# Kernel optimization log

Measured on AMD Instinct MI355X. Metric: run time of the kernel, lower is better.

The kernel has to match this reference:

```python
import jax, jax.numpy as jnp
import numpy as np

SIGMA = 25.0
EPS = 1e-5
TWO_PI = 2.0 * np.pi


def _gn(x, gamma, beta, groups):
    # GroupNorm over (C//G, H, W) per group, per-channel affine.
    B, C, H, W = x.shape
    xg = x.reshape(B, groups, -1)
    m = xg.mean(-1, keepdims=True)
    v = xg.var(-1, keepdims=True)
    xn = ((xg - m) * jax.lax.rsqrt(v + EPS)).reshape(B, C, H, W)
    return xn * gamma[None, :, None, None] + beta[None, :, None, None]


def _conv3(x, k, b):
    y = jax.lax.conv_general_dilated(x, k, (1, 1), 'SAME',
                                     dimension_numbers=('NCHW', 'OIHW', 'NCHW'))
    return y + b[None, :, None, None]


def _tconv2(x, k, b):
    # ConvTranspose2d kernel=2 stride=2 (no overlap) == einsum + reshape.
    # k: [C_in, C_out, 2, 2]
    B, C, H, W = x.shape
    O = k.shape[1]
    y = jnp.einsum('bchw,codq->bohdwq', x, k).reshape(B, O, 2 * H, 2 * W)
    return y + b[None, :, None, None]


def _conv1(x, k, b):
    # 1x1 conv; k: [C_out, C_in]
    return jnp.einsum('bchw,oc->bohw', x, k) + b[None, :, None, None]


def _pool(x):
    B, C, H, W = x.shape
    return x.reshape(B, C, H // 2, 2, W // 2, 2).max(axis=(3, 5))


def _std(t):
    return jnp.sqrt((SIGMA ** (2.0 * t) - 1.0) / (2.0 * jnp.log(SIGMA)))


def setup_inputs() -> dict:
    key = jax.random.key(0)
    ks = jax.random.split(key, 16)
    B, H, W = 64, 128, 128
    E = 2 * W  # 256 = embed_dim

    def w(k, shape, fan_in):
        return jax.random.normal(k, shape, jnp.float32) / np.sqrt(fan_in)

    inp = {
        'x': jax.random.normal(ks[0], (B, 1, H, W), jnp.float32),
        't': jax.random.uniform(ks[1], (B,), jnp.float32, 1e-3, 1.0),
        'Wf': jax.random.normal(ks[2], (H, W), jnp.float32) * 30.0,  # fixed Fourier features
        'fc1_w': w(ks[3], (E, E), E),
        'fc1_b': jnp.zeros((E,), jnp.float32),
        'conv1_k': w(ks[4], (6, 1, 3, 3), 9),
        'conv1_b': jnp.zeros((6,), jnp.float32),
        'gn1_g': jnp.ones((6,), jnp.float32), 'gn1_b': jnp.zeros((6,), jnp.float32),
        'conv2_k': w(ks[5], (24, 6, 3, 3), 6 * 9),
        'conv2_b': jnp.zeros((24,), jnp.float32),
        'gn2_g': jnp.ones((24,), jnp.float32), 'gn2_b': jnp.zeros((24,), jnp.float32),
        't3_k': w(ks[6], (24, 24, 2, 2), 24 * 4),
        't3_b': jnp.zeros((24,), jnp.float32),
        'gn3_g': jnp.ones((48,), jnp.float32), 'gn3_b': jnp.zeros((48,), jnp.float32),
        't4_k': w(ks[7], (48, 12, 2, 2), 48 * 4),
        't4_b': jnp.zeros((12,), jnp.float32),
        'gn4_g': jnp.ones((18,), jnp.float32), 'gn4_b': jnp.zeros((18,), jnp.float32),
        't5_k': w(ks[8], (6, 18), 18),
        't5_b': jnp.zeros((6,), jnp.float32),
        'gn5_g': jnp.ones((6,), jnp.float32), 'gn5_b': jnp.zeros((6,), jnp.float32),
        'fin_k': w(ks[9], (1, 6), 6),
        'fin_b': jnp.zeros((1,), jnp.float32),
    }
    return inp


def reference(x, t, Wf, fc1_w, fc1_b, conv1_k, conv1_b, gn1_g, gn1_b,
              conv2_k, conv2_b, gn2_g, gn2_b, t3_k, t3_b, gn3_g, gn3_b,
              t4_k, t4_b, gn4_g, gn4_b, t5_k, t5_b, gn5_g, gn5_b,
              fin_k, fin_b):
    # Vectorized Gaussian Fourier projection: [B,1,H,W] -> [B,1,H,2W]
    p = x * Wf[None, None] * TWO_PI
    xe = jnp.concatenate([jnp.sin(p), jnp.cos(p)], axis=-1)
    # fc1 on last dim (embed_dim = 2W)
    xf = jnp.einsum('bchw,ow->bcho', xe, fc1_w) + fc1_b
    c1 = _conv3(xf, conv1_k, conv1_b)                              # [B,6,H,2W]
    p1 = _pool(jax.nn.relu(_gn(c1, gn1_g, gn1_b, 6)))              # [B,6,H/2,W]
    c2 = _conv3(p1, conv2_k, conv2_b)                              # [B,24,H/2,W]
    p2 = _pool(jax.nn.relu(_gn(c2, gn2_g, gn2_b, 24)))             # [B,24,H/4,W/2]
    a = p2 * jax.nn.sigmoid(p2)                                    # SiLU bottleneck
    u3 = _tconv2(a, t3_k, t3_b)                                    # [B,24,H/2,W]
    g3 = _gn(jnp.concatenate([c2, u3], axis=1), gn3_g, gn3_b, 6)   # 48 ch
    u4 = _tconv2(g3, t4_k, t4_b)                                   # [B,12,H,2W]
    g4 = _gn(jnp.concatenate([c1, u4], axis=1), gn4_g, gn4_b, 6)   # 18 ch
    u5 = _conv1(g4, t5_k, t5_b)                                    # [B,6,H,2W]
    g5 = _gn(u5, gn5_g, gn5_b, 6)
    return _conv1(g5, fin_k, fin_b) / _std(t)[:, None, None, None]
```

## Files before the change

### kernel.cpp

```cpp
#include <hip/hip_runtime.h>
#include <hip/hip_bf16.h>
#include <math.h>

#define BB 64
#define HH 128
#define WW 128
#define EE 256
#define HP (HH*EE)
#define H2 64
#define W2 128
#define PL2 (H2*W2)
#define H4 32
#define W4 64
#define PL4 (H4*W4)

typedef __hip_bfloat16 bf;
typedef unsigned short ushortt;
typedef __attribute__((ext_vector_type(8))) __bf16 b8v;
typedef __attribute__((ext_vector_type(4))) float f4v;

__device__ __forceinline__ float tof(bf v)    { return __bfloat162float(v); }
__device__ __forceinline__ bf    tob(float v) { return __float2bfloat16(v); }
__device__ __forceinline__ unsigned int bfbits(float v) {
    return (unsigned int)__builtin_bit_cast(ushortt, __float2bfloat16(v));
}
__device__ __forceinline__ float b2f(unsigned int u16) {
    unsigned int x = u16 << 16;
    return __builtin_bit_cast(float, x);
}
__device__ __forceinline__ void wred2(float& s, float& q) {
    #pragma unroll
    for (int m = 32; m; m >>= 1) {
        s += __shfl_xor(s, m);
        q += __shfl_xor(q, m);
    }
}

__global__ __launch_bounds__(256) void k_fourier_fc1(
    const float* __restrict__ x, const float* __restrict__ Wf,
    const float* __restrict__ fc1_w, const float* __restrict__ fc1_b,
    bf* __restrict__ xf, float* __restrict__ mb)
{
    __shared__ ushortt sA[64*264];
    __shared__ ushortt sB[64*264];
    int t = threadIdx.x;
    for (int i = blockIdx.x*256 + t; i < 9280; i += 512*256) mb[i] = 0.f;
    int rb = blockIdx.x >> 2, cb = blockIdx.x & 3;
    int row0 = rb*64, col0 = cb*64;
    const float TP = 6.2831853071795864769f;
    for (int it = 0; it < 32; ++it) {
        int i = it*256 + t;
        int r = i >> 7, w = i & 127;
        int rg = row0 + r;
        float p = x[(size_t)rg*WW + w] * Wf[(size_t)(rg & (HH-1))*WW + w] * TP;
        sA[r*264 + w]       = (ushortt)bfbits(__sinf(p));
        sA[r*264 + 128 + w] = (ushortt)bfbits(__cosf(p));
    }
    #pragma unroll
    for (int it = 0; it < 16; ++it) {
        int i = it*256 + t;
        int o = i >> 6, c4 = i & 63;
        float4 w4 = *(const float4*)(fc1_w + (size_t)(col0 + o)*EE + c4*4);
        uint2 pk;
        pk.x = bfbits(w4.x) | (bfbits(w4.y) << 16);
        pk.y = bfbits(w4.z) | (bfbits(w4.w) << 16);
        *(uint2*)&sB[o*264 + c4*4] = pk;
    }
    __syncthreads();
    int lane = t & 63, wid = t >> 6;
    int m = lane & 15, kq = (lane >> 4) * 8;
    f4v acc[4] = {};
    const ushortt* aBase = &sA[(wid*16 + m)*264 + kq];
    #pragma unroll
    for (int k0 = 0; k0 < 8; ++k0) {
        b8v av = *(const b8v*)(aBase + k0*32);
        #pragma unroll
        for (int t4 = 0; t4 < 4; ++t4) {
            b8v bv = *(const b8v*)&sB[(t4*16 + m)*264 + k0*32 + kq];
            acc[t4] = __builtin_amdgcn_mfma_f32_16x16x32_bf16(av, bv, acc[t4], 0, 0, 0);
        }
    }
    int rbase = row0 + wid*16 + (lane >> 4)*4;
    #pragma unroll
    for (int t4 = 0; t4 < 4; ++t4) {
        int col = col0 + t4*16 + m;
        float bias = fc1_b[col];
        #pragma unroll
        for (int r = 0; r < 4; ++r)
            xf[(size_t)(rbase + r)*EE + col] = tob(acc[t4][r] + bias);
    }
}

__global__ __launch_bounds__(256) void k_conv1(
    const bf* __restrict__ xf, const float* __restrict__ k,
    const float* __restrict__ bias, bf* __restrict__ c1, float* __restrict__ mc1)
{
    __shared__ ushortt sT[6*272];
    __shared__ float red[4][6][2];
    int t = threadIdx.x;
    int bid = ((blockIdx.x & 7) << 8) | (blockIdx.x >> 3);
    int ht = bid & 31, b = bid >> 5;
    int h0 = ht*4;
    const bf* src = xf + (size_t)b*HP;
    if (t < 192) {
        int r = t >> 5, i = t & 31;
        int gy = h0 - 1 + r;
        uint4 v = {0,0,0,0};
        if (gy >= 0 && gy < HH) v = *(const uint4*)(src + (size_t)gy*EE + i*8);
        *(uint4*)&sT[r*272 + 8 + i*8] = v;
    } else if (t < 204) {
        int e = t - 192;
        int r = e >> 1, s = e & 1;
        uint4 z = {0,0,0,0};
        *(uint4*)&sT[r*272 + s*264] = z;
    }
    __syncthreads();
    int wq = (t & 63)*4, hl = t >> 6;
    int lane = t & 63, wid = t >> 6;
    float v[3][6];
    #pragma unroll
    for (int ky = 0; ky < 3; ++ky)
      #pragma unroll
      for (int j = 0; j < 6; ++j)
        v[ky][j] = b2f((unsigned)sT[(hl+ky)*272 + 7 + wq + j]);
    int h = h0 + hl;
    #pragma unroll
    for (int o = 0; o < 6; ++o) {
        float bv = bias[o];
        float a0=bv, a1=bv, a2=bv, a3=bv;
        #pragma unroll
        for (int ky = 0; ky < 3; ++ky)
          #pragma unroll
          for (int kx = 0; kx < 3; ++kx) {
            float wv = k[o*9 + ky*3 + kx];
            a0 += v[ky][kx+0]*wv;
            a1 += v[ky][kx+1]*wv;
            a2 += v[ky][kx+2]*wv;
            a3 += v[ky][kx+3]*wv;
          }
        uint2 pk;
        pk.x = bfbits(a0) | (bfbits(a1) << 16);
        pk.y = bfbits(a2) | (bfbits(a3) << 16);
        *(uint2*)(c1 + ((size_t)(b*6+o)*HH + h)*EE + wq) = pk;
        float s = a0+a1+a2+a3, q = a0*a0+a1*a1+a2*a2+a3*a3;
        wred2(s, q);
        if (lane == 0) { red[wid][o][0] = s; red[wid][o][1] = q; }
    }
    __syncthreads();
    if (t < 6) {
        float S = 0.f, Q = 0.f;
        #pragma unroll
        for (int wv = 0; wv < 4; ++wv) { S += red[wv][t][0]; Q += red[wv][t][1]; }
        atomicAdd(&mc1[((size_t)b*6 + t)*2],     S);
        atomicAdd(&mc1[((size_t)b*6 + t)*2 + 1], Q);
    }
}

__global__ __launch_bounds__(256) void k_conv2(
    const bf* __restrict__ c1, const float* __restrict__ mc1,
    const float* __restrict__ g1, const float* __restrict__ be1,
    const float* __restrict__ kw, const float* __restrict__ bias,
    bf* __restrict__ c2, float* __restrict__ mc2)
{
    __shared__ ushortt sA[256*64];
    __shared__ ushortt sW[32*64];
    __shared__ ushortt sP[6*4*136];
    __shared__ float ssl[12];
    __shared__ float redS[24], redQ[24];
    int t = threadIdx.x;
    int bid = ((blockIdx.x & 7) << 8) | (blockIdx.x >> 3);
    int ht = bid & 31, b = bid >> 5;
    int h0 = ht*2;
    int lane = t & 63, wid = t >> 6;
    int m = lane & 15, q4 = lane >> 4;
    if (t < 24) { redS[t] = 0.f; redQ[t] = 0.f; }
    if (t < 6) {
        float s = mc1[((size_t)b*6 + t)*2], q = mc1[((size_t)b*6 + t)*2 + 1];
        float mean = s * (1.f/HP);
        float var  = q * (1.f/HP) - mean*mean;
        float rstd = rsqrtf(var + 1e-5f);
        float sc = g1[t]*rstd;
        ssl[t*2] = sc; ssl[t*2+1] = be1[t] - mean*sc;
    }
    for (int i = t; i < 1024; i += 256) ((unsigned*)sW)[i] = 0;
    if (t < 48) {
        int c = t >> 3, e = t & 7;
        int ry = e >> 1, rx = (e & 1) ? 129 : 0;
        sP[c*544 + ry*136 + rx] = 0;
    }
    __syncthreads();
    #pragma unroll
    for (int j = 0; j < 12; ++j) {
        int i = j*256 + t;
        int c = i >> 9, ry = (i >> 7) & 3, gx = i & 127;
        int gy = h0 - 1 + ry;
        float v = 0.f;
        if (gy >= 0 && gy < H2) {
            const bf* pp = c1 + ((size_t)(b*6+c)*HH + 2*gy)*EE + 2*gx;
            unsigned r0 = *(const unsigned*)pp;
            unsigned r1 = *(const unsigned*)(pp + EE);
            float sc = ssl[c*2], sh = ssl[c*2+1];
            float e0 = fmaxf(b2f(r0 & 0xffff)*sc+sh, 0.f);
            float e1 = fmaxf(b2f(r0 >> 16)   *sc+sh, 0.f);
            float e2 = fmaxf(b2f(r1 & 0xffff)*sc+sh, 0.f);
            float e3 = fmaxf(b2f(r1 >> 16)   *sc+sh, 0.f);
            v = fmaxf(fmaxf(e0,e1), fmaxf(e2,e3));
        }
        sP[c*544 + ry*136 + gx + 1] = (ushortt)bfbits(v);
    }
    #pragma unroll
    for (int j = 0; j < 6; ++j) {
        int i = j*256 + t;
        int o = i >> 6, kk = i & 63;
        if (kk < 54)
            sW[o*64 + ((((kk >> 3) ^ (o & 7)) << 3) | (kk & 7))] =
                (ushortt)bfbits(kw[o*54 + kk]);
    }
    __syncthreads();
    {
        int r = t >> 7, xx = t & 127;
        unsigned u[32];
        #pragma unroll
        for (int p = 0; p < 27; ++p) {
            int k0 = 2*p, k1 = 2*p + 1;
            int c0 = k0/9, y0 = (k0%9)/3, x0 = k0%3;
            int c1i = k1/9, y1 = (k1%9)/3, x1 = k1%3;
            unsigned lo = sP[c0*544 + (r+y0)*136 + xx + x0];
            unsigned hi = sP[c1i*544 + (r+y1)*136 + xx + x1];
            u[p] = lo | (hi << 16);
        }
        #pragma unroll
        for (int p = 27; p < 32; ++p) u[p] = 0;
        #pragma unroll
        for (int e = 0; e < 8; ++e) {
            uint4 pk; pk.x = u[4*e]; pk.y = u[4*e+1]; pk.z = u[4*e+2]; pk.w = u[4*e+3];
            *(uint4*)&sA[t*64 + ((e ^ (t & 7)) << 3)] = pk;
        }
    }
    __syncthreads();
    b8v wv[2][2];
    #pragma unroll
    for (int nt = 0; nt < 2; ++nt) {
        int o = nt*16 + m;
        #pragma unroll
        for (int ks = 0; ks < 2; ++ks)
            wv[nt][ks] = *(const b8v*)&sW[o*64 + (((ks*4 + q4) ^ (o & 7)) << 3)];
    }
    f4v acc[4][2] = {};
    #pragma unroll
    for (int mt = 0; mt < 4; ++mt) {
        int px = wid*64 + mt*16 + m;
        b8v a0 = *(const b8v*)&sA[px*64 + (((q4)     ^ (px & 7)) << 3)];
        b8v a1 = *(const b8v*)&sA[px*64 + (((4 + q4) ^ (px & 7)) << 3)];
        #pragma unroll
        for (int nt = 0; nt < 2; ++nt) {
            acc[mt][nt] = __builtin_amdgcn_mfma_f32_16x16x32_bf16(a0, wv[nt][0], acc[mt][nt], 0, 0, 0);
            acc[mt][nt] = __builtin_amdgcn_mfma_f32_16x16x32_bf16(a1, wv[nt][1], acc[mt][nt], 0, 0, 0);
        }
    }
    float sAcc[2] = {0.f, 0.f}, qAcc[2] = {0.f, 0.f};
    #pragma unroll
    for (int nt = 0; nt < 2; ++nt) {
        int o = nt*16 + m;
        bool valid = (o < 24);
        float bo = valid ? bias[o] : 0.f;
        #pragma unroll
        for (int mt = 0; mt < 4; ++mt) {
            int pxb = wid*64 + mt*16 + q4*4;
            unsigned l0 = bfbits(acc[mt][nt][0] + bo);
            unsigned l1 = bfbits(acc[mt][nt][1] + bo);
            unsigned l2 = bfbits(acc[mt][nt][2] + bo);
            unsigned l3 = bfbits(acc[mt][nt][3] + bo);
            if (valid) {
                uint2 pk; pk.x = l0 | (l1 << 16); pk.y = l2 | (l3 << 16);
                int r = pxb >> 7, xx = pxb & 127;
                *(uint2*)(c2 + ((size_t)(b*24+o))*PL2 + (size_t)(h0 + r)*W2 + xx) = pk;
                float f0 = b2f(l0), f1 = b2f(l1), f2 = b2f(l2), f3 = b2f(l3);
                sAcc[nt] += f0+f1+f2+f3;
                qAcc[nt] += f0*f0+f1*f1+f2*f2+f3*f3;
            }
        }
    }
    #pragma unroll
    for (int nt = 0; nt < 2; ++nt) {
        int o = nt*16 + m;
        float s = sAcc[nt], q = qAcc[nt];
        s += __shfl_xor(s, 16); q += __shfl_xor(q, 16);
        s += __shfl_xor(s, 32); q += __shfl_xor(q, 32);
        if (q4 == 0 && o < 24) { atomicAdd(&redS[o], s); atomicAdd(&redQ[o], q); }
    }
    __syncthreads();
    if (t < 24) {
        atomicAdd(&mc2[((size_t)b*24 + t)*2],     redS[t]);
        atomicAdd(&mc2[((size_t)b*24 + t)*2 + 1], redQ[t]);
    }
}

__global__ __launch_bounds__(256) void k_tconv3(
    const bf* __restrict__ c2, const float* __restrict__ mc2,
    const float* __restrict__ g2, const float* __restrict__ be2,
    const float* __restrict__ k3, const float* __restrict__ b3,
    bf* __restrict__ u3, float* __restrict__ mu3)
{
    __shared__ ushortt sA[128*64];
    __shared__ ushortt sW[96*64];
    __shared__ float redS[24], redQ[24];
    __shared__ float ssl[48];
    int t = threadIdx.x;
    int b = blockIdx.x >> 4, pg = blockIdx.x & 15;
    int lane = t & 63, wid = t >> 6;
    int m = lane & 15, q4 = lane >> 4;
    if (t < 24) {
        redS[t] = 0.f; redQ[t] = 0.f;
        float s = mc2[((size_t)b*24 + t)*2], q = mc2[((size_t)b*24 + t)*2 + 1];
        float mean = s * (1.f/PL2);
        float var  = q * (1.f/PL2) - mean*mean;
        float rstd = rsqrtf(var + 1e-5f);
        float sc = g2[t]*rstd;
        ssl[t*2] = sc; ssl[t*2+1] = be2[t] - mean*sc;
    }
    if (t < 96) {
        uint4 z = {0,0,0,0};
        *(uint4*)&sW[t*64 + (((3 ^ (t & 3)) + (t & 4)) << 3)] = z;
    }
    #pragma unroll
    for (int j = 0; j < 12; ++j) {
        int i = j*256 + t;
        int c = i >> 7, n = i & 127;
        if (n < 96)
            sW[n*64 + (((((c >> 3) ^ (n & 3)) + (n & 4)) << 3) | (c & 7))] =
                (ushortt)bfbits(k3[c*96 + n]);
    }
    {
        int px = t & 127, half = t >> 7;
        int pix = pg*128 + px;
        int h4 = pix >> 6, w4 = pix & 63;
        const bf* base = c2 + (size_t)b*24*PL2 + (size_t)(2*h4)*W2 + 2*w4;
        auto stageG = [&](int g) {
            unsigned pr[4];
            #pragma unroll
            for (int hc = 0; hc < 4; ++hc) {
                unsigned two[2];
                #pragma unroll
                for (int cc = 0; cc < 2; ++cc) {
                    int c = g*8 + hc*2 + cc;
                    const bf* pp = base + (size_t)c*PL2;
                    unsigned r0 = *(const unsigned*)pp;
                    unsigned r1 = *(const unsigned*)(pp + W2);
                    float sc = ssl[c*2], sh = ssl[c*2+1];
                    float e0 = fmaxf(b2f(r0 & 0xffff)*sc+sh, 0.f);
                    float e1 = fmaxf(b2f(r0 >> 16)   *sc+sh, 0.f);
                    float e2 = fmaxf(b2f(r1 & 0xffff)*sc+sh, 0.f);
                    float e3 = fmaxf(b2f(r1 >> 16)   *sc+sh, 0.f);
                    float mm = fmaxf(fmaxf(e0,e1), fmaxf(e2,e3));
                    mm = mm / (1.f + __expf(-mm));
                    two[cc] = bfbits(mm);
                }
                pr[hc] = two[0] | (two[1] << 16);
            }
            uint4 pk; pk.x = pr[0]; pk.y = pr[1]; pk.z = pr[2]; pk.w = pr[3];
            *(uint4*)&sA[px*64 + (((g ^ (px & 3)) + (px & 4)) << 3)] = pk;
        };
        if (half == 0) {
            stageG(0);
            stageG(1);
        } else {
            stageG(2);
            uint4 z = {0,0,0,0};
            *(uint4*)&sA[px*64 + (((3 ^ (px & 3)) + (px & 4)) << 3)] = z;
        }
    }
    __syncthreads();
    b8v wv[6];
    #pragma unroll
    for (int nt = 0; nt < 6; ++nt) {
        int n = nt*16 + m;
        wv[nt] = *(const b8v*)&sW[n*64 + (((q4 ^ (n & 3)) + (n & 4)) << 3)];
    }
    f4v acc[2][6] = {};
    #pragma unroll
    for (int mt = 0; mt < 2; ++mt) {
        int px = wid*32 + mt*16 + m;
        b8v av = *(const b8v*)&sA[px*64 + (((q4 ^ (px & 3)) + (px & 4)) << 3)];
        #pragma unroll
        for (int nt = 0; nt < 6; ++nt)
            acc[mt][nt] = __builtin_amdgcn_mfma_f32_16x16x32_bf16(av, wv[nt], acc[mt][nt], 0, 0, 0);
    }
    float sAcc[6] = {}, qAcc[6] = {};
    int qq = m & 1;
    #pragma unroll
    for (int nt = 0; nt < 6; ++nt) {
        int n = nt*16 + m;
        int o = n >> 2, d = (n >> 1) & 1;
        float bo = b3[o];
        #pragma unroll
        for (int mt = 0; mt < 2; ++mt) {
            int pxb = wid*32 + mt*16 + q4*4;
            unsigned wds[4];
            float s = 0.f, q = 0.f;
            #pragma unroll
            for (int r = 0; r < 4; ++r) {
                float v = acc[mt][nt][r] + bo;
                float vp = __shfl_xor(v, 1);
                unsigned lo = bfbits(v), hi = bfbits(vp);
                wds[r] = lo | (hi << 16);
                float f0 = b2f(lo), f1 = b2f(hi);
                s += f0 + f1;
                q += f0*f0 + f1*f1;
            }
            if (qq == 0) {
                int pix = pg*128 + pxb;
                int h4 = pix >> 6;
                int w4 = pix & 63;
                uint4 pk; pk.x = wds[0]; pk.y = wds[1]; pk.z = wds[2]; pk.w = wds[3];
                *(uint4*)(u3 + ((size_t)(b*24 + o))*PL2 + (size_t)(2*h4 + d)*W2 + 2*w4) = pk;
                sAcc[nt] += s; qAcc[nt] += q;
            }
        }
    }
    #pragma unroll
    for (int nt = 0; nt < 6; ++nt) {
        float s = sAcc[nt], q = qAcc[nt];
        s += __shfl_xor(s, 2);  q += __shfl_xor(q, 2);
        s += __shfl_xor(s, 16); q += __shfl_xor(q, 16);
        s += __shfl_xor(s, 32); q += __shfl_xor(q, 32);
        if ((lane & 51) == 0) {
            int o = nt*4 + (m >> 2);
            atomicAdd(&redS[o], s);
            atomicAdd(&redQ[o], q);
        }
    }
    __syncthreads();
    if (t < 24) {
        atomicAdd(&mu3[((size_t)b*24 + t)*2],     redS[t]);
        atomicAdd(&mu3[((size_t)b*24 + t)*2 + 1], redQ[t]);
    }
}

__global__ __launch_bounds__(256) void k_tconv4(
    const bf* __restrict__ c2, const bf* __restrict__ u3,
    const float* __restrict__ mc2, const float* __restrict__ mu3,
    const float* __restrict__ g3, const float* __restrict__ be3,
    const float* __restrict__ k4, const float* __restrict__ bias4,
    bf* __restrict__ u4, float* __restrict__ mu4)
{
    __shared__ ushortt sA[256*64];
    __shared__ ushortt sW[48*64];
    __shared__ float redS[12], redQ[12];
    __shared__ float ssl[96];
    int t = threadIdx.x;
    int b = blockIdx.x >> 5, pg = blockIdx.x & 31;
    int lane = t & 63, wid = t >> 6;
    int m = lane & 15, q4 = lane >> 4;
    if (t < 12) { redS[t] = 0.f; redQ[t] = 0.f; }
    if (t < 6) {
        float s = 0.f, q = 0.f;
        #pragma unroll
        for (int cl = 0; cl < 8; ++cl) {
            int gc = t*8 + cl;
            const float* p = (gc < 24) ? mc2 + ((size_t)b*24 + gc)*2
                                       : mu3 + ((size_t)b*24 + gc - 24)*2;
            s += p[0]; q += p[1];
        }
        float inv_n = 1.f/((float)PL2*8.f);
        float mean = s*inv_n;
        float var  = q*inv_n - mean*mean;
        float rstd = rsqrtf(var + 1e-5f);
        #pragma unroll
        for (int cl = 0; cl < 8; ++cl) {
            int gc = t*8 + cl;
            float sc = g3[gc]*rstd;
            ssl[gc*2] = sc; ssl[gc*2+1] = be3[gc] - mean*sc;
        }
    }
    #pragma unroll
    for (int j = 0; j < 12; ++j) {
        int i = j*256 + t;
        int c = i >> 6, n = i & 63;
        if (n < 48)
            sW[n*64 + ((((c >> 3) ^ (n & 7)) << 3) | (c & 7))] =
                (ushortt)bfbits(k4[c*48 + n]);
    }
    if (t < 96) {
        uint4 z = {0,0,0,0};
        int n = t >> 1, kb = 6 + (t & 1);
        *(uint4*)&sW[n*64 + ((kb ^ (n & 7)) << 3)] = z;
    }
    {
        int px = t;
        int pix = pg*256 + px;
        const bf* c2p = c2 + (size_t)b*24*PL2 + pix;
        const bf* u3p = u3 + (size_t)b*24*PL2 + pix;
        #pragma unroll
        for (int g = 0; g < 6; ++g) {
            unsigned pr[4];
            #pragma unroll
            for (int hc = 0; hc < 4; ++hc) {
                int c0 = g*8 + hc*2;
                float r0 = (c0 < 24) ? tof(c2p[(size_t)c0*PL2]) : tof(u3p[(size_t)(c0-24)*PL2]);
                float r1 = (c0+1 < 24) ? tof(c2p[(size_t)(c0+1)*PL2]) : tof(u3p[(size_t)(c0+1-24)*PL2]);
                float v0 = r0 * ssl[2*c0]   + ssl[2*c0+1];
                float v1 = r1 * ssl[2*c0+2] + ssl[2*c0+3];
                pr[hc] = bfbits(v0) | (bfbits(v1) << 16);
            }
            uint4 pk; pk.x = pr[0]; pk.y = pr[1]; pk.z = pr[2]; pk.w = pr[3];
            *(uint4*)&sA[px*64 + ((g ^ (px & 7)) << 3)] = pk;
        }
        uint4 z = {0,0,0,0};
        *(uint4*)&sA[px*64 + ((6 ^ (px & 7)) << 3)] = z;
        *(uint4*)&sA[px*64 + ((7 ^ (px & 7)) << 3)] = z;
    }
    __syncthreads();
    b8v bfr[3][2];
    #pragma unroll
    for (int nt = 0; nt < 3; ++nt) {
        int n = nt*16 + m;
        #pragma unroll
        for (int ks = 0; ks < 2; ++ks)
            bfr[nt][ks] = *(const b8v*)&sW[n*64 + (((ks*4 + q4) ^ (n & 7)) << 3)];
    }
    f4v acc[4][3] = {};
    #pragma unroll
    for (int mt = 0; mt < 4; ++mt) {
        int px = wid*64 + mt*16 + m;
        b8v a0 = *(const b8v*)&sA[px*64 + (((q4)     ^ (px & 7)) << 3)];
        b8v a1 = *(const b8v*)&sA[px*64 + (((4 + q4) ^ (px & 7)) << 3)];
        #pragma unroll
        for (int nt = 0; nt < 3; ++nt) {
            acc[mt][nt] = __builtin_amdgcn_mfma_f32_16x16x32_bf16(a0, bfr[nt][0], acc[mt][nt], 0, 0, 0);
            acc[mt][nt] = __builtin_amdgcn_mfma_f32_16x16x32_bf16(a1, bfr[nt][1], acc[mt][nt], 0, 0, 0);
        }
    }
    float sAcc[3] = {0.f, 0.f, 0.f}, qAcc[3] = {0.f, 0.f, 0.f};
    int qq = m & 1;
    #pragma unroll
    for (int nt = 0; nt < 3; ++nt) {
        int n = nt*16 + m;
        int o = n >> 2, d = (n >> 1) & 1;
        float bo = bias4[o];
        #pragma unroll
        for (int mt = 0; mt < 4; ++mt) {
            int pxb = wid*64 + mt*16 + q4*4;
            unsigned wds[4];
            float s = 0.f, q = 0.f;
            #pragma unroll
            for (int r = 0; r < 4; ++r) {
                float v = acc[mt][nt][r] + bo;
                float vp = __shfl_xor(v, 1);
                unsigned lo = bfbits(v), hi = bfbits(vp);
                wds[r] = lo | (hi << 16);
                float f0 = b2f(lo), f1 = b2f(hi);
                s += f0 + f1;
                q += f0*f0 + f1*f1;
            }
            if (qq == 0) {
                int h2 = (pg*256 + pxb) >> 7;
                int w0 = pxb & 127;
                uint4 pk; pk.x = wds[0]; pk.y = wds[1]; pk.z = wds[2]; pk.w = wds[3];
                *(uint4*)(u4 + (((size_t)(b*12 + o))*HH + 2*h2 + d)*EE + 2*w0) = pk;
                sAcc[nt] += s; qAcc[nt] += q;
            }
        }
    }
    #pragma unroll
    for (int nt = 0; nt < 3; ++nt) {
        float s = sAcc[nt], q = qAcc[nt];
        s += __shfl_xor(s, 2);  q += __shfl_xor(q, 2);
        s += __shfl_xor(s, 16); q += __shfl_xor(q, 16);
        s += __shfl_xor(s, 32); q += __shfl_xor(q, 32);
        if ((lane & 51) == 0) {
            int o = nt*4 + (m >> 2);
            atomicAdd(&redS[o], s);
            atomicAdd(&redQ[o], q);
        }
    }
    __syncthreads();
    if (t < 12) {
        atomicAdd(&mu4[((size_t)b*12 + t)*2],     redS[t]);
        atomicAdd(&mu4[((size_t)b*12 + t)*2 + 1], redQ[t]);
    }
}

__global__ __launch_bounds__(256) void k_conv1x1_u5(
    const bf* __restrict__ c1, const bf* __restrict__ u4,
    const float* __restrict__ mc1, const float* __restrict__ mu4,
    const float* __restrict__ g4, const float* __restrict__ be4,
    const float* __restrict__ k, const float* __restrict__ bias,
    bf* __restrict__ u5, float* __restrict__ mu5)
{
    __shared__ float red[4][6][2];
    __shared__ float ssl[36];
    int t = threadIdx.x;
    int b  = blockIdx.x >> 4;
    int pg = blockIdx.x & 15;
    int pix = pg*2048 + t*8;
    int lane = t & 63, wid = t >> 6;
    if (t < 6) {
        float s = 0.f, q = 0.f;
        #pragma unroll
        for (int cl = 0; cl < 3; ++cl) {
            int gc = t*3 + cl;
            const float* p = (gc < 6) ? mc1 + ((size_t)b*6 + gc)*2
                                      : mu4 + ((size_t)b*12 + gc - 6)*2;
            s += p[0]; q += p[1];
        }
        float inv_n = 1.f/((float)HP*3.f);
        float mean = s*inv_n;
        float var  = q*inv_n - mean*mean;
        float rstd = rsqrtf(var + 1e-5f);
        #pragma unroll
        for (int cl = 0; cl < 3; ++cl) {
            int gc = t*3 + cl;
            float sc = g4[gc]*rstd;
            ssl[gc*2] = sc; ssl[gc*2+1] = be4[gc] - mean*sc;
        }
    }
    __syncthreads();
    const bf* c1p = c1 + ((size_t)b*6)*HP + pix;
    const bf* u4p = u4 + ((size_t)b*12)*HP + pix;
    float acc[6][8];
    #pragma unroll
    for (int o = 0; o < 6; ++o) {
        float bv = bias[o];
        #pragma unroll
        for (int j = 0; j < 8; ++j) acc[o][j] = bv;
    }
    #pragma unroll
    for (int c = 0; c < 18; ++c) {
        uint4 r = (c < 6) ? *(const uint4*)(c1p + (size_t)c*HP)
                          : *(const uint4*)(u4p + (size_t)(c-6)*HP);
        float sc = ssl[2*c], sh = ssl[2*c+1];
        float v[8];
        v[0] = b2f(r.x & 0xffff)*sc + sh;  v[1] = b2f(r.x >> 16)*sc + sh;
        v[2] = b2f(r.y & 0xffff)*sc + sh;  v[3] = b2f(r.y >> 16)*sc + sh;
        v[4] = b2f(r.z & 0xffff)*sc + sh;  v[5] = b2f(r.z >> 16)*sc + sh;
        v[6] = b2f(r.w & 0xffff)*sc + sh;  v[7] = b2f(r.w >> 16)*sc + sh;
        #pragma unroll
        for (int o = 0; o < 6; ++o) {
            float wv = k[o*18 + c];
            #pragma unroll
            for (int j = 0; j < 8; ++j) acc[o][j] += v[j]*wv;
        }
    }
    #pragma unroll
    for (int o = 0; o < 6; ++o) {
        uint4 pk;
        pk.x = bfbits(acc[o][0]) | (bfbits(acc[o][1]) << 16);
        pk.y = bfbits(acc[o][2]) | (bfbits(acc[o][3]) << 16);
        pk.z = bfbits(acc[o][4]) | (bfbits(acc[o][5]) << 16);
        pk.w = bfbits(acc[o][6]) | (bfbits(acc[o][7]) << 16);
        *(uint4*)(u5 + ((size_t)(b*6+o))*HP + pix) = pk;
        float s = 0.f, q = 0.f;
        #pragma unroll
        for (int j = 0; j < 8; ++j) { s += acc[o][j]; q += acc[o][j]*acc[o][j]; }
        wred2(s, q);
        if (lane == 0) { red[wid][o][0] = s; red[wid][o][1] = q; }
    }
    __syncthreads();
    if (t < 6) {
        float S = 0.f, Q = 0.f;
        #pragma unroll
        for (int wv = 0; wv < 4; ++wv) { S += red[wv][t][0]; Q += red[wv][t][1]; }
        atomicAdd(&mu5[((size_t)b*6 + t)*2],     S);
        atomicAdd(&mu5[((size_t)b*6 + t)*2 + 1], Q);
    }
}

__global__ __launch_bounds__(256) void k_final(
    const bf* __restrict__ u5, const float* __restrict__ mu5,
    const float* __restrict__ g5, const float* __restrict__ be5,
    const float* __restrict__ k, const float* __restrict__ bias,
    const float* __restrict__ t, float* __restrict__ out)
{
    __shared__ float ssl[12];
    int tt = threadIdx.x;
    int b = blockIdx.x >> 4;
    int pix = ((blockIdx.x & 15)*256 + tt)*8;
    if (tt < 6) {
        float s = mu5[((size_t)b*6 + tt)*2], q = mu5[((size_t)b*6 + tt)*2 + 1];
        float mean = s * (1.f/HP);
        float var  = q * (1.f/HP) - mean*mean;
        float rstd = rsqrtf(var + 1e-5f);
        float sc = g5[tt]*rstd;
        ssl[tt*2] = sc; ssl[tt*2+1] = be5[tt] - mean*sc;
    }
    __syncthreads();
    const bf* up = u5 + (size_t)b*6*HP + pix;
    float bv = bias[0];
    float a[8];
    #pragma unroll
    for (int j = 0; j < 8; ++j) a[j] = bv;
    #pragma unroll
    for (int c = 0; c < 6; ++c) {
        uint4 r = *(const uint4*)(up + (size_t)c*HP);
        float sc = ssl[2*c], sh = ssl[2*c+1];
        float wv = k[c];
        a[0] += (b2f(r.x & 0xffff)*sc + sh) * wv;
        a[1] += (b2f(r.x >> 16)   *sc + sh) * wv;
        a[2] += (b2f(r.y & 0xffff)*sc + sh) * wv;
        a[3] += (b2f(r.y >> 16)   *sc + sh) * wv;
        a[4] += (b2f(r.z & 0xffff)*sc + sh) * wv;
        a[5] += (b2f(r.z >> 16)   *sc + sh) * wv;
        a[6] += (b2f(r.w & 0xffff)*sc + sh) * wv;
        a[7] += (b2f(r.w >> 16)   *sc + sh) * wv;
    }
    float tb = t[b];
    const float lns = 3.2188758248682007492f;
    float var = (expf(2.f*tb*lns) - 1.f) / (2.f*lns);
    float rs = rsqrtf(var);
    float4 o0; o0.x = a[0]*rs; o0.y = a[1]*rs; o0.z = a[2]*rs; o0.w = a[3]*rs;
    float4 o1; o1.x = a[4]*rs; o1.y = a[5]*rs; o1.z = a[6]*rs; o1.w = a[7]*rs;
    float* op = out + (size_t)b*HP + pix;
    *(float4*)op       = o0;
    *(float4*)(op + 4) = o1;
}

extern "C" void kernel_launch(void* const* d_in, const int* in_sizes, int n_in,
                              void* d_out, int out_size, void* d_ws, size_t ws_size,
                              hipStream_t stream)
{
    const float* x       = (const float*)d_in[0];
    const float* t       = (const float*)d_in[1];
    const float* Wf      = (const float*)d_in[2];
    const float* fc1_w   = (const float*)d_in[3];
    const float* fc1_b   = (const float*)d_in[4];
    const float* conv1_k = (const float*)d_in[5];
    const float* conv1_b = (const float*)d_in[6];
    const float* gn1_g   = (const float*)d_in[7];
    const float* gn1_b   = (const float*)d_in[8];
    const float* conv2_k = (const float*)d_in[9];
    const float* conv2_b = (const float*)d_in[10];
    const float* gn2_g   = (const float*)d_in[11];
    const float* gn2_b   = (const float*)d_in[12];
    const float* t3_k    = (const float*)d_in[13];
    const float* t3_b    = (const float*)d_in[14];
    const float* gn3_g   = (const float*)d_in[15];
    const float* gn3_b   = (const float*)d_in[16];
    const float* t4_k    = (const float*)d_in[17];
    const float* t4_b    = (const float*)d_in[18];
    const float* gn4_g   = (const float*)d_in[19];
    const float* gn4_b   = (const float*)d_in[20];
    const float* t5_k    = (const float*)d_in[21];
    const float* t5_b    = (const float*)d_in[22];
    const float* gn5_g   = (const float*)d_in[23];
    const float* gn5_b   = (const float*)d_in[24];
    const float* fin_k   = (const float*)d_in[25];
    const float* fin_b   = (const float*)d_in[26];

    bf* wsb = (bf*)d_ws;
    bf* c1 = wsb;
    bf* c2 = wsb + 12582912;
    bf* u3 = wsb + 25165824;
    bf* u4 = wsb + 37748736;
    bf* xf = wsb + 39845888;
    bf* u5 = wsb + 12582912;
    float* mb = (float*)(wsb + 62914560);
    float* mc1 = mb;
    float* mc2 = mb + 768;
    float* mu3 = mb + 3840;
    float* mu4 = mb + 6912;
    float* mu5 = mb + 8448;

    k_fourier_fc1<<<512, 256, 0, stream>>>(x, Wf, fc1_w, fc1_b, xf, mb);
    k_conv1<<<2048, 256, 0, stream>>>(xf, conv1_k, conv1_b, c1, mc1);
    k_conv2<<<2048, 256, 0, stream>>>(c1, mc1, gn1_g, gn1_b,
                                      conv2_k, conv2_b, c2, mc2);
    k_tconv3<<<1024, 256, 0, stream>>>(c2, mc2, gn2_g, gn2_b,
                                       t3_k, t3_b, u3, mu3);
    k_tconv4<<<2048, 256, 0, stream>>>(c2, u3, mc2, mu3, gn3_g, gn3_b,
                                       t4_k, t4_b, u4, mu4);
    k_conv1x1_u5<<<1024, 256, 0, stream>>>(c1, u4, mc1, mu4, gn4_g, gn4_b,
                                           t5_k, t5_b, u5, mu5);
    k_final<<<1024, 256, 0, stream>>>(u5, mu5, gn5_g, gn5_b,
                                      fin_k, fin_b, t, (float*)d_out);
}
```

Baseline: 228.7 us.

## Build MFMA A-operand fragments directly in registers instead of staging through LDS

In the conv2, tconv3 and tconv4 kernels, the im2col/activation tile is no longer written to a shared-memory sA buffer and read back. Each lane now gathers its own MFMA A fragment straight from sP or global memory into registers, which removes an LDS round trip, one barrier, and a large shared allocation that limited occupancy. In exchange, each lane issues scattered 2-byte loads in the MFMA lane layout, and global reads become less coalesced because they are strided by channel.

```diff
diff --git a/kernel.cpp b/kernel.cpp
--- a/kernel.cpp
+++ b/kernel.cpp
@@ -162,7 +162,6 @@
     const float* __restrict__ kw, const float* __restrict__ bias,
     bf* __restrict__ c2, float* __restrict__ mc2)
 {
-    __shared__ ushortt sA[256*64];
     __shared__ ushortt sW[32*64];
     __shared__ ushortt sP[6*4*136];
     __shared__ float ssl[12];
@@ -217,27 +216,6 @@
                 (ushortt)bfbits(kw[o*54 + kk]);
     }
     __syncthreads();
-    {
-        int r = t >> 7, xx = t & 127;
-        unsigned u[32];
-        #pragma unroll
-        for (int p = 0; p < 27; ++p) {
-            int k0 = 2*p, k1 = 2*p + 1;
-            int c0 = k0/9, y0 = (k0%9)/3, x0 = k0%3;
-            int c1i = k1/9, y1 = (k1%9)/3, x1 = k1%3;
-            unsigned lo = sP[c0*544 + (r+y0)*136 + xx + x0];
-            unsigned hi = sP[c1i*544 + (r+y1)*136 + xx + x1];
-            u[p] = lo | (hi << 16);
-        }
-        #pragma unroll
-        for (int p = 27; p < 32; ++p) u[p] = 0;
-        #pragma unroll
-        for (int e = 0; e < 8; ++e) {
-            uint4 pk; pk.x = u[4*e]; pk.y = u[4*e+1]; pk.z = u[4*e+2]; pk.w = u[4*e+3];
-            *(uint4*)&sA[t*64 + ((e ^ (t & 7)) << 3)] = pk;
-        }
-    }
-    __syncthreads();
     b8v wv[2][2];
     #pragma unroll
     for (int nt = 0; nt < 2; ++nt) {
@@ -246,12 +224,41 @@
         for (int ks = 0; ks < 2; ++ks)
             wv[nt][ks] = *(const b8v*)&sW[o*64 + (((ks*4 + q4) ^ (o & 7)) << 3)];
     }
+    int offA0[8], offA1[8];
+    #pragma unroll
+    for (int j = 0; j < 8; ++j) {
+        int k0 = q4*8 + j;
+        int c = (k0*57) >> 9;
+        int r9 = k0 - 9*c;
+        int y = (r9*11) >> 5;
+        int xk = r9 - 3*y;
+        offA0[j] = c*544 + y*136 + xk;
+        int k1 = 32 + q4*8 + j;
+        c = (k1*57) >> 9;
+        r9 = k1 - 9*c;
+        y = (r9*11) >> 5;
+        xk = r9 - 3*y;
+        offA1[j] = (k1 < 54) ? (c*544 + y*136 + xk) : -1;
+    }
     f4v acc[4][2] = {};
     #pragma unroll
     for (int mt = 0; mt < 4; ++mt) {
         int px = wid*64 + mt*16 + m;
-        b8v a0 = *(const b8v*)&sA[px*64 + (((q4)     ^ (px & 7)) << 3)];
-        b8v a1 = *(const b8v*)&sA[px*64 + (((4 + q4) ^ (px & 7)) << 3)];
+        int badd = (px >> 7)*136 + (px & 127);
+        unsigned w0[4], w1[4];
+        #pragma unroll
+        for (int jj = 0; jj < 4; ++jj) {
+            unsigned lo  = sP[offA0[2*jj]   + badd];
+            unsigned hi  = sP[offA0[2*jj+1] + badd];
+            w0[jj] = lo | (hi << 16);
+            unsigned lo1 = (offA1[2*jj]   >= 0) ? (unsigned)sP[offA1[2*jj]   + badd] : 0u;
+            unsigned hi1 = (offA1[2*jj+1] >= 0) ? (unsigned)sP[offA1[2*jj+1] + badd] : 0u;
+            w1[jj] = lo1 | (hi1 << 16);
+        }
+        uint4 u0; u0.x = w0[0]; u0.y = w0[1]; u0.z = w0[2]; u0.w = w0[3];
+        uint4 u1; u1.x = w1[0]; u1.y = w1[1]; u1.z = w1[2]; u1.w = w1[3];
+        b8v a0 = __builtin_bit_cast(b8v, u0);
+        b8v a1 = __builtin_bit_cast(b8v, u1);
         #pragma unroll
         for (int nt = 0; nt < 2; ++nt) {
             acc[mt][nt] = __builtin_amdgcn_mfma_f32_16x16x32_bf16(a0, wv[nt][0], acc[mt][nt], 0, 0, 0);
@@ -302,7 +309,6 @@
     const float* __restrict__ k3, const float* __restrict__ b3,
     bf* __restrict__ u3, float* __restrict__ mu3)
 {
-    __shared__ ushortt sA[128*64];
     __shared__ ushortt sW[96*64];
     __shared__ float redS[24], redQ[24];
     __shared__ float ssl[48];
@@ -331,19 +337,29 @@
             sW[n*64 + (((((c >> 3) ^ (n & 3)) + (n & 4)) << 3) | (c & 7))] =
                 (ushortt)bfbits(k3[c*96 + n]);
     }
-    {
-        int px = t & 127, half = t >> 7;
+    __syncthreads();
+    b8v wv[6];
+    #pragma unroll
+    for (int nt = 0; nt < 6; ++nt) {
+        int n = nt*16 + m;
+        wv[nt] = *(const b8v*)&sW[n*64 + (((q4 ^ (n & 3)) + (n & 4)) << 3)];
+    }
+    f4v acc[2][6] = {};
+    #pragma unroll
+    for (int mt = 0; mt < 2; ++mt) {
+        int px = wid*32 + mt*16 + m;
         int pix = pg*128 + px;
         int h4 = pix >> 6, w4 = pix & 63;
         const bf* base = c2 + (size_t)b*24*PL2 + (size_t)(2*h4)*W2 + 2*w4;
-        auto stageG = [&](int g) {
+        uint4 au = {0,0,0,0};
+        if (q4 < 3) {
             unsigned pr[4];
             #pragma unroll
-            for (int hc = 0; hc < 4; ++hc) {
+            for (int jj = 0; jj < 4; ++jj) {
                 unsigned two[2];
                 #pragma unroll
                 for (int cc = 0; cc < 2; ++cc) {
-                    int c = g*8 + hc*2 + cc;
+                    int c = q4*8 + jj*2 + cc;
                     const bf* pp = base + (size_t)c*PL2;
                     unsigned r0 = *(const unsigned*)pp;
                     unsigned r1 = *(const unsigned*)(pp + W2);
@@ -356,32 +372,11 @@
                     mm = mm / (1.f + __expf(-mm));
                     two[cc] = bfbits(mm);
                 }
-                pr[hc] = two[0] | (two[1] << 16);
+                pr[jj] = two[0] | (two[1] << 16);
             }
-            uint4 pk; pk.x = pr[0]; pk.y = pr[1]; pk.z = pr[2]; pk.w = pr[3];
-            *(uint4*)&sA[px*64 + (((g ^ (px & 3)) + (px & 4)) << 3)] = pk;
-        };
-        if (half == 0) {
-            stageG(0);
-            stageG(1);
-        } else {
-            stageG(2);
-            uint4 z = {0,0,0,0};
-            *(uint4*)&sA[px*64 + (((3 ^ (px & 3)) + (px & 4)) << 3)] = z;
-        }
-    }
-    __syncthreads();
-    b8v wv[6];
-    #pragma unroll
-    for (int nt = 0; nt < 6; ++nt) {
-        int n = nt*16 + m;
-        wv[nt] = *(const b8v*)&sW[n*64 + (((q4 ^ (n & 3)) + (n & 4)) << 3)];
-    }
-    f4v acc[2][6] = {};
-    #pragma unroll
-    for (int mt = 0; mt < 2; ++mt) {
-        int px = wid*32 + mt*16 + m;
-        b8v av = *(const b8v*)&sA[px*64 + (((q4 ^ (px & 3)) + (px & 4)) << 3)];
+            au.x = pr[0]; au.y = pr[1]; au.z = pr[2]; au.w = pr[3];
+        }
+        b8v av = __builtin_bit_cast(b8v, au);
         #pragma unroll
         for (int nt = 0; nt < 6; ++nt)
             acc[mt][nt] = __builtin_amdgcn_mfma_f32_16x16x32_bf16(av, wv[nt], acc[mt][nt], 0, 0, 0);
@@ -444,7 +439,6 @@
     const float* __restrict__ k4, const float* __restrict__ bias4,
     bf* __restrict__ u4, float* __restrict__ mu4)
 {
-    __shared__ ushortt sA[256*64];
     __shared__ ushortt sW[48*64];
     __shared__ float redS[12], redQ[12];
     __shared__ float ssl[96];
@@ -486,30 +480,6 @@
         int n = t >> 1, kb = 6 + (t & 1);
         *(uint4*)&sW[n*64 + ((kb ^ (n & 7)) << 3)] = z;
     }
-    {
-        int px = t;
-        int pix = pg*256 + px;
-        const bf* c2p = c2 + (size_t)b*24*PL2 + pix;
-        const bf* u3p = u3 + (size_t)b*24*PL2 + pix;
-        #pragma unroll
-        for (int g = 0; g < 6; ++g) {
-            unsigned pr[4];
-            #pragma unroll
-            for (int hc = 0; hc < 4; ++hc) {
-                int c0 = g*8 + hc*2;
-                float r0 = (c0 < 24) ? tof(c2p[(size_t)c0*PL2]) : tof(u3p[(size_t)(c0-24)*PL2]);
-                float r1 = (c0+1 < 24) ? tof(c2p[(size_t)(c0+1)*PL2]) : tof(u3p[(size_t)(c0+1-24)*PL2]);
-                float v0 = r0 * ssl[2*c0]   + ssl[2*c0+1];
-                float v1 = r1 * ssl[2*c0+2] + ssl[2*c0+3];
-                pr[hc] = bfbits(v0) | (bfbits(v1) << 16);
-            }
-            uint4 pk; pk.x = pr[0]; pk.y = pr[1]; pk.z = pr[2]; pk.w = pr[3];
-            *(uint4*)&sA[px*64 + ((g ^ (px & 7)) << 3)] = pk;
-        }
-        uint4 z = {0,0,0,0};
-        *(uint4*)&sA[px*64 + ((6 ^ (px & 7)) << 3)] = z;
-        *(uint4*)&sA[px*64 + ((7 ^ (px & 7)) << 3)] = z;
-    }
     __syncthreads();
     b8v bfr[3][2];
     #pragma unroll
@@ -523,8 +493,43 @@
     #pragma unroll
     for (int mt = 0; mt < 4; ++mt) {
         int px = wid*64 + mt*16 + m;
-        b8v a0 = *(const b8v*)&sA[px*64 + (((q4)     ^ (px & 7)) << 3)];
-        b8v a1 = *(const b8v*)&sA[px*64 + (((4 + q4) ^ (px & 7)) << 3)];
+        int pix = pg*256 + px;
+        const ushortt* pc2 = (const ushortt*)c2 + (size_t)b*24*PL2 + pix;
+        const ushortt* pu3 = (const ushortt*)u3 + (size_t)b*24*PL2 + pix;
+        unsigned pr[4];
+        #pragma unroll
+        for (int jj = 0; jj < 4; ++jj) {
+            unsigned two[2];
+            #pragma unroll
+            for (int cc = 0; cc < 2; ++cc) {
+                int c = q4*8 + jj*2 + cc;
+                unsigned raw = (c < 24) ? (unsigned)pc2[(size_t)c*PL2]
+                                        : (unsigned)pu3[(size_t)(c-24)*PL2];
+                float v = b2f(raw)*ssl[2*c] + ssl[2*c+1];
+                two[cc] = bfbits(v);
+            }
+            pr[jj] = two[0] | (two[1] << 16);
+        }
+        uint4 u0; u0.x = pr[0]; u0.y = pr[1]; u0.z = pr[2]; u0.w = pr[3];
+        b8v a0 = __builtin_bit_cast(b8v, u0);
+        uint4 u1 = {0,0,0,0};
+        if (q4 < 2) {
+            unsigned pr1[4];
+            #pragma unroll
+            for (int jj = 0; jj < 4; ++jj) {
+                unsigned two[2];
+                #pragma unroll
+                for (int cc = 0; cc < 2; ++cc) {
+                    int c = 32 + q4*8 + jj*2 + cc;
+                    unsigned raw = (unsigned)pu3[(size_t)(c-24)*PL2];
+                    float v = b2f(raw)*ssl[2*c] + ssl[2*c+1];
+                    two[cc] = bfbits(v);
+                }
+                pr1[jj] = two[0] | (two[1] << 16);
+            }
+            u1.x = pr1[0]; u1.y = pr1[1]; u1.z = pr1[2]; u1.w = pr1[3];
+        }
+        b8v a1 = __builtin_bit_cast(b8v, u1);
         #pragma unroll
         for (int nt = 0; nt < 3; ++nt) {
             acc[mt][nt] = __builtin_amdgcn_mfma_f32_16x16x32_bf16(a0, bfr[nt][0], acc[mt][nt], 0, 0, 0);
```

After: 227.1 us. No clear change (-0.7%).
